# Performance work log

Measured on AMD Instinct MI355X. Metric: run time of the kernel, lower is better.

## Reference

```python
import jax, jax.numpy as jnp
import numpy as np

NEG_SLOPE = 0.2


def gat_conv(x, src, dst, W, att_src, att_dst, bias, heads, out_ch):
    # x: [N, Fin]; src/dst: [E] (self-loops already included)
    N = x.shape[0]
    h = (x @ W).reshape(N, heads, out_ch)                      # [N, H, C]
    a_s = jnp.einsum('nhc,hc->nh', h, att_src)                 # [N, H]
    a_d = jnp.einsum('nhc,hc->nh', h, att_dst)                 # [N, H]
    e = jax.nn.leaky_relu(a_s[src] + a_d[dst], NEG_SLOPE)      # [E, H]
    # segment softmax over incoming edges of each dst node
    e_max = jax.ops.segment_max(e, dst, num_segments=N)        # [N, H]
    p = jnp.exp(e - e_max[dst])                                # [E, H]
    denom = jax.ops.segment_sum(p, dst, num_segments=N)        # [N, H]
    alpha = p / denom[dst]                                     # [E, H]
    msg = h[src] * alpha[:, :, None]                           # [E, H, C]
    out = jax.ops.segment_sum(msg, dst, num_segments=N)        # [N, H, C]
    return out.reshape(N, heads * out_ch) + bias


def setup_inputs() -> dict:
    key = jax.random.key(0)
    ks = jax.random.split(key, 10)
    N, E, F_IN, HID, HEADS, NCLS = 100000, 3200000, 512, 8, 8, 16
    x = jax.random.normal(ks[0], (N, F_IN), dtype=jnp.float32)
    edge_index = jax.random.randint(ks[1], (2, E), 0, N, dtype=jnp.int64)
    s = 1.0 / np.sqrt(F_IN)
    W1 = jax.random.uniform(ks[2], (F_IN, HEADS * HID), jnp.float32, -s, s)
    att_src1 = jax.random.normal(ks[3], (HEADS, HID), jnp.float32) * 0.1
    att_dst1 = jax.random.normal(ks[4], (HEADS, HID), jnp.float32) * 0.1
    b1 = jnp.zeros((HEADS * HID,), jnp.float32)
    s2 = 1.0 / np.sqrt(HEADS * HID)
    W2 = jax.random.uniform(ks[5], (HEADS * HID, NCLS), jnp.float32, -s2, s2)
    att_src2 = jax.random.normal(ks[6], (1, NCLS), jnp.float32) * 0.1
    att_dst2 = jax.random.normal(ks[7], (1, NCLS), jnp.float32) * 0.1
    b2 = jnp.zeros((NCLS,), jnp.float32)
    return {"x": x, "edge_index": edge_index, "W1": W1, "att_src1": att_src1,
            "att_dst1": att_dst1, "b1": b1, "W2": W2, "att_src2": att_src2,
            "att_dst2": att_dst2, "b2": b2}


def reference(x, edge_index, W1, att_src1, att_dst1, b1, W2, att_src2, att_dst2, b2):
    N = x.shape[0]
    loops = jnp.arange(N, dtype=edge_index.dtype)
    src = jnp.concatenate([edge_index[0], loops])  # PyG add_self_loops=True
    dst = jnp.concatenate([edge_index[1], loops])
    # eval mode: F.dropout is identity
    h = gat_conv(x, src, dst, W1, att_src1, att_dst1, b1, heads=8, out_ch=8)
    h = jax.nn.elu(h)
    out = gat_conv(h, src, dst, W2, att_src2, att_dst2, b2, heads=1, out_ch=16)
    return out
```

## Files before the change

kernel.cpp:

```cpp
#include <hip/hip_runtime.h>

#define F_IN 512
#define F1 64
#define NCLS 16
#define NEG_SLOPE 0.2f

typedef __attribute__((ext_vector_type(8))) short short8;
typedef __attribute__((ext_vector_type(4))) float f32x4;

__device__ __forceinline__ unsigned short f2bf(float f) {
    unsigned u = __float_as_uint(f);
    return (unsigned short)((u + 0x7fffu + ((u >> 16) & 1u)) >> 16);
}
__device__ __forceinline__ float bf2f(unsigned short u) {
    return __uint_as_float(((unsigned)u) << 16);
}


__global__ __launch_bounds__(64) void k_detect(const int* __restrict__ ei, int E,
                                               unsigned* __restrict__ mode) {
    int t = threadIdx.x;
    unsigned nz = 0;
    int lim = (E > 256) ? 256 : E;
    for (int k = t; k < lim; k += 64) nz |= (unsigned)ei[2 * k + 1];
    for (int off = 1; off < 64; off <<= 1) nz |= __shfl_xor(nz, off);
    if (t == 0) *mode = (nz == 0) ? 1u : 0u;
}

__device__ __forceinline__ void decode_edge(const int* __restrict__ ei,
                                            const long long* __restrict__ e64,
                                            bool m64, unsigned i, int E, int N,
                                            int& s, int& v) {
    if (i < (unsigned)E) {
        if (m64) { s = (int)e64[i]; v = (int)e64[E + i]; }
        else     { s = ei[i];       v = ei[E + i]; }
    } else {
        s = (int)(i - (unsigned)E);
        v = s;
    }
    s = s < 0 ? 0 : (s >= N ? N - 1 : s);
    v = v < 0 ? 0 : (v >= N ? N - 1 : v);
}

__device__ __forceinline__ int decode_dst(const int* __restrict__ ei,
                                          const long long* __restrict__ e64,
                                          bool m64, unsigned i, int E, int N) {
    int v;
    if (i < (unsigned)E) v = m64 ? (int)e64[E + i] : ei[E + i];
    else                 v = (int)(i - (unsigned)E);
    return v < 0 ? 0 : (v >= N ? N - 1 : v);
}


__device__ __forceinline__ void gemm1_tile(const float* __restrict__ x,
                                           const float* __restrict__ W1,
                                           const float* __restrict__ att_s,
                                           const float* __restrict__ att_d,
                                           unsigned short* __restrict__ h1b,
                                           float* __restrict__ a_s1,
                                           float* __restrict__ a_d1,
                                           int N, int row0,
                                           unsigned short (*Abuf)[40],
                                           unsigned short (*BbufT)[40]) {
    const int tid = threadIdx.x;
    const int w = tid >> 6, lane = tid & 63;
    const int quad = lane >> 4, r16 = lane & 15;

    f32x4 acc[4];
#pragma unroll
    for (int t = 0; t < 4; t++) acc[t] = (f32x4){0.f, 0.f, 0.f, 0.f};

    const int a_row = tid >> 2;
    const int a_seg = (tid & 3) * 8;
    const int b_col = tid & 63;
    const int b_kq  = tid >> 6;
    const int ar = row0 + a_row;

    for (int k0 = 0; k0 < F_IN; k0 += 32) {
        {
            float4 v0 = make_float4(0.f, 0.f, 0.f, 0.f), v1 = v0;
            if (ar < N) {
                const float* xp = x + (size_t)ar * F_IN + k0 + a_seg;
                v0 = *(const float4*)xp;
                v1 = *(const float4*)(xp + 4);
            }
            short8 cv;
            cv[0] = (short)f2bf(v0.x); cv[1] = (short)f2bf(v0.y);
            cv[2] = (short)f2bf(v0.z); cv[3] = (short)f2bf(v0.w);
            cv[4] = (short)f2bf(v1.x); cv[5] = (short)f2bf(v1.y);
            cv[6] = (short)f2bf(v1.z); cv[7] = (short)f2bf(v1.w);
            *(short8*)&Abuf[a_row][a_seg] = cv;
        }
        {
            const float* wp = W1 + (size_t)(k0 + b_kq * 8) * F1 + b_col;
            short8 cv;
#pragma unroll
            for (int j = 0; j < 8; j++)
                cv[j] = (short)f2bf(wp[(size_t)j * F1]);
            *(short8*)&BbufT[b_col][b_kq * 8] = cv;
        }
        __syncthreads();

        short8 af = *(const short8*)&Abuf[w * 16 + r16][quad * 8];
#pragma unroll
        for (int t = 0; t < 4; t++) {
            short8 bf = *(const short8*)&BbufT[t * 16 + r16][quad * 8];
            acc[t] = __builtin_amdgcn_mfma_f32_16x16x32_bf16(af, bf, acc[t], 0, 0, 0);
        }
        __syncthreads();
    }

    float ats[4], atd[4];
#pragma unroll
    for (int t = 0; t < 4; t++) {
        ats[t] = att_s[t * 16 + r16];
        atd[t] = att_d[t * 16 + r16];
    }
#pragma unroll
    for (int r = 0; r < 4; r++) {
        int grow = row0 + w * 16 + quad * 4 + r;
        bool ok = grow < N;
        float ps[4], pd[4];
#pragma unroll
        for (int t = 0; t < 4; t++) {
            float vv = acc[t][r];
            if (ok) h1b[(size_t)grow * F1 + t * 16 + r16] = f2bf(vv);
            ps[t] = vv * ats[t];
            pd[t] = vv * atd[t];
        }
#pragma unroll
        for (int t = 0; t < 4; t++) {
            ps[t] += __shfl_xor(ps[t], 1); pd[t] += __shfl_xor(pd[t], 1);
            ps[t] += __shfl_xor(ps[t], 2); pd[t] += __shfl_xor(pd[t], 2);
            ps[t] += __shfl_xor(ps[t], 4); pd[t] += __shfl_xor(pd[t], 4);
        }
        if (ok && (r16 & 7) == 0) {
            int hh0 = r16 >> 3;
#pragma unroll
            for (int t = 0; t < 4; t++) {
                a_s1[(size_t)grow * 8 + t * 2 + hh0] = ps[t];
                a_d1[(size_t)grow * 8 + t * 2 + hh0] = pd[t];
            }
        }
    }
}


__global__ __launch_bounds__(256) void k_fusedA(const float* __restrict__ x,
                                                const float* __restrict__ W1,
                                                const float* __restrict__ att_s,
                                                const float* __restrict__ att_d,
                                                unsigned short* __restrict__ h1b,
                                                float* __restrict__ a_s1,
                                                float* __restrict__ a_d1, int N,
                                                const int* __restrict__ ei,
                                                const unsigned* __restrict__ mode,
                                                unsigned* __restrict__ bucketCnt,
                                                int E, int ET, int nch,
                                                int nb, int shift) {
    __shared__ __align__(16) char smem[10240];
    unsigned b = blockIdx.x;
    if ((b & 1) == 0) {
        gemm1_tile(x, W1, att_s, att_d, h1b, a_s1, a_d1, N, (int)(b >> 1) * 64,
                   (unsigned short (*)[40])smem,
                   (unsigned short (*)[40])(smem + 5120));
        return;
    }
    unsigned* cntL = (unsigned*)smem;
    for (int i = threadIdx.x; i < 1024; i += 256) cntL[i] = 0u;
    __syncthreads();

    const unsigned stride = (unsigned)nch * 256u;
    bool m64 = (*mode != 0u);
    const long long* e64 = (const long long*)ei;
    unsigned i = (b >> 1) * 256u + threadIdx.x;
    for (; i + 3u * stride < (unsigned)ET; i += 4u * stride) {
        int v0 = decode_dst(ei, e64, m64, i, E, N);
        int v1 = decode_dst(ei, e64, m64, i + stride, E, N);
        int v2 = decode_dst(ei, e64, m64, i + 2u * stride, E, N);
        int v3 = decode_dst(ei, e64, m64, i + 3u * stride, E, N);
        atomicAdd(&cntL[(unsigned)v0 >> shift], 1u);
        atomicAdd(&cntL[(unsigned)v1 >> shift], 1u);
        atomicAdd(&cntL[(unsigned)v2 >> shift], 1u);
        atomicAdd(&cntL[(unsigned)v3 >> shift], 1u);
    }
    for (; i < (unsigned)ET; i += stride) {
        int v = decode_dst(ei, e64, m64, i, E, N);
        atomicAdd(&cntL[(unsigned)v >> shift], 1u);
    }
    __syncthreads();
    for (int k = threadIdx.x; k < nb; k += 256) {
        unsigned c = cntL[k];
        if (c) atomicAdd(&bucketCnt[k], c);
    }
}


__global__ __launch_bounds__(256) void k_fusedB(const float* __restrict__ x,
                                                const float* __restrict__ W1,
                                                const float* __restrict__ att_s,
                                                const float* __restrict__ att_d,
                                                unsigned short* __restrict__ h1b,
                                                float* __restrict__ a_s1,
                                                float* __restrict__ a_d1, int N,
                                                int rowSplit,
                                                const int* __restrict__ ei,
                                                const unsigned* __restrict__ mode,
                                                unsigned* __restrict__ bucketFill,
                                                unsigned* __restrict__ pairs,
                                                int E, int ET, int nch,
                                                int nb, int shift) {
    __shared__ __align__(16) char smem[10240];
    unsigned b = blockIdx.x;
    if (b & 1) {
        gemm1_tile(x, W1, att_s, att_d, h1b, a_s1, a_d1, N,
                   rowSplit + (int)(b >> 1) * 64,
                   (unsigned short (*)[40])smem,
                   (unsigned short (*)[40])(smem + 5120));
        return;
    }
    unsigned* cntA = (unsigned*)smem;
    unsigned* ofsA = (unsigned*)(smem + 4096);
    unsigned* part = (unsigned*)(smem + 8192);
    const int t = threadIdx.x;
    const int chunk = (ET + nch - 1) / nch;
    const int cbase = (int)(b >> 1) * chunk;
    const int cend = (cbase + chunk < ET) ? cbase + chunk : ET;
    const unsigned lmask = (1u << shift) - 1u;
    bool m64 = (*mode != 0u);
    const long long* e64 = (const long long*)ei;

    for (int k = t; k < 1024; k += 256) cntA[k] = 0u;
    __syncthreads();
    for (int k = cbase + t; k < cend; k += 256) {
        int v = decode_dst(ei, e64, m64, (unsigned)k, E, N);
        atomicAdd(&cntA[(unsigned)v >> shift], 1u);
    }
    __syncthreads();
    unsigned a0 = cntA[4 * t + 0], a1 = cntA[4 * t + 1];
    unsigned a2 = cntA[4 * t + 2], a3 = cntA[4 * t + 3];
    unsigned ssum = a0 + a1 + a2 + a3;
    part[t] = ssum;
    __syncthreads();
    for (int off = 1; off < 256; off <<= 1) {
        unsigned add = (t >= off) ? part[t - off] : 0u;
        __syncthreads();
        part[t] += add;
        __syncthreads();
    }
    unsigned excl = part[t] - ssum;
    ofsA[4 * t + 0] = excl;
    ofsA[4 * t + 1] = excl + a0;
    ofsA[4 * t + 2] = excl + a0 + a1;
    ofsA[4 * t + 3] = excl + a0 + a1 + a2;
    __syncthreads();
    for (int k = t; k < nb; k += 256) {
        unsigned c = cntA[k];
        unsigned g = c ? atomicAdd(&bucketFill[k], c) : 0u;
        cntA[k] = g - ofsA[k];
    }
    __syncthreads();
    for (int k = cbase + t; k < cend; k += 256) {
        int s, v;
        decode_edge(ei, e64, m64, (unsigned)k, E, N, s, v);
        unsigned bb = (unsigned)v >> shift;
        unsigned slot = atomicAdd(&ofsA[bb], 1u);
        pairs[cntA[bb] + slot] = (unsigned)s | (((unsigned)v & lmask) << 20);
    }
}


__global__ __launch_bounds__(1024) void k_scan_buckets(const unsigned* __restrict__ bucketCnt,
                                                       int nb, int ET,
                                                       unsigned* __restrict__ bucketOfs,
                                                       unsigned* __restrict__ bucketFill,
                                                       unsigned* __restrict__ row_ptr,
                                                       int N) {
    __shared__ unsigned sbuf[1024];
    int t = threadIdx.x;
    unsigned val = (t < nb) ? bucketCnt[t] : 0u;
    sbuf[t] = val;
    __syncthreads();
    for (int off = 1; off < 1024; off <<= 1) {
        unsigned add = (t >= off) ? sbuf[t - off] : 0u;
        __syncthreads();
        sbuf[t] += add;
        __syncthreads();
    }
    if (t < nb) {
        unsigned e = sbuf[t] - val;
        bucketOfs[t] = e;
        bucketFill[t] = e;
    }
    if (t == 0) row_ptr[N] = (unsigned)ET;
}


__global__ __launch_bounds__(256) void k_sort(const unsigned* __restrict__ pairs,
                                              const unsigned* __restrict__ bucketOfs,
                                              const unsigned* __restrict__ bucketCnt,
                                              unsigned* __restrict__ row_ptr,
                                              unsigned* __restrict__ ssrc,
                                              int N, int shift) {
    __shared__ unsigned f[1024];
    __shared__ unsigned part[256];
    const int b = blockIdx.x;
    const int t = threadIdx.x;
    const int nodes = 1 << shift;
    const int bbase = b << shift;
    for (int i = t; i < 1024; i += 256) f[i] = 0u;
    __syncthreads();
    const unsigned base = bucketOfs[b];
    const unsigned cnt = bucketCnt[b];
    for (unsigned i = (unsigned)t; i < cnt; i += 256u)
        atomicAdd(&f[pairs[base + i] >> 20], 1u);
    __syncthreads();
    unsigned a0 = f[4 * t + 0], a1 = f[4 * t + 1];
    unsigned a2 = f[4 * t + 2], a3 = f[4 * t + 3];
    unsigned ssum = a0 + a1 + a2 + a3;
    part[t] = ssum;
    __syncthreads();
    for (int off = 1; off < 256; off <<= 1) {
        unsigned add = (t >= off) ? part[t - off] : 0u;
        __syncthreads();
        part[t] += add;
        __syncthreads();
    }
    unsigned excl = part[t] - ssum;
    unsigned c0 = base + excl;
    unsigned c1 = c0 + a0;
    unsigned c2 = c1 + a1;
    unsigned c3 = c2 + a2;
    {
        int v0 = bbase + 4 * t;
        if (v0 + 0 < N && 4 * t + 0 < nodes) row_ptr[v0 + 0] = c0;
        if (v0 + 1 < N && 4 * t + 1 < nodes) row_ptr[v0 + 1] = c1;
        if (v0 + 2 < N && 4 * t + 2 < nodes) row_ptr[v0 + 2] = c2;
        if (v0 + 3 < N && 4 * t + 3 < nodes) row_ptr[v0 + 3] = c3;
    }
    f[4 * t + 0] = c0;
    f[4 * t + 1] = c1;
    f[4 * t + 2] = c2;
    f[4 * t + 3] = c3;
    __syncthreads();
    for (unsigned i = (unsigned)t; i < cnt; i += 256u) {
        unsigned pk = pairs[base + i];
        unsigned local = pk >> 20;
        unsigned pos = atomicAdd(&f[local], 1u);
        ssrc[pos] = pk & 0xFFFFFu;
    }
}


__global__ __launch_bounds__(256) void k_agg1(const unsigned short* __restrict__ h1b,
                                              const float* __restrict__ a_s1,
                                              const float* __restrict__ a_d1,
                                              const float* __restrict__ b1,
                                              const unsigned* __restrict__ row_ptr,
                                              const unsigned* __restrict__ ssrc,
                                              float* __restrict__ g, int N) {
    int wid = threadIdx.x >> 6, lane = threadIdx.x & 63;
    int v = blockIdx.x * 4 + wid;
    if (v >= N) return;
    unsigned base = row_ptr[v];
    unsigned deg = row_ptr[v + 1] - base;
    int h = lane >> 3;
    float adv = a_d1[(size_t)v * 8 + h];

    float denom = 0.f, acc = 0.f;
    unsigned j = 0;
    for (; j + 8 <= deg; j += 8) {
        unsigned s0 = ssrc[base + j + 0];
        unsigned s1 = ssrc[base + j + 1];
        unsigned s2 = ssrc[base + j + 2];
        unsigned s3 = ssrc[base + j + 3];
        unsigned s4 = ssrc[base + j + 4];
        unsigned s5 = ssrc[base + j + 5];
        unsigned s6 = ssrc[base + j + 6];
        unsigned s7 = ssrc[base + j + 7];
        float as0 = a_s1[(size_t)s0 * 8 + h];
        float as1 = a_s1[(size_t)s1 * 8 + h];
        float as2 = a_s1[(size_t)s2 * 8 + h];
        float as3 = a_s1[(size_t)s3 * 8 + h];
        float as4 = a_s1[(size_t)s4 * 8 + h];
        float as5 = a_s1[(size_t)s5 * 8 + h];
        float as6 = a_s1[(size_t)s6 * 8 + h];
        float as7 = a_s1[(size_t)s7 * 8 + h];
        float h0 = bf2f(h1b[(size_t)s0 * F1 + lane]);
        float h1 = bf2f(h1b[(size_t)s1 * F1 + lane]);
        float h2v = bf2f(h1b[(size_t)s2 * F1 + lane]);
        float h3 = bf2f(h1b[(size_t)s3 * F1 + lane]);
        float h4 = bf2f(h1b[(size_t)s4 * F1 + lane]);
        float h5 = bf2f(h1b[(size_t)s5 * F1 + lane]);
        float h6 = bf2f(h1b[(size_t)s6 * F1 + lane]);
        float h7 = bf2f(h1b[(size_t)s7 * F1 + lane]);
        float e0 = as0 + adv; e0 = e0 > 0.f ? e0 : NEG_SLOPE * e0; float p0 = __expf(e0);
        float e1 = as1 + adv; e1 = e1 > 0.f ? e1 : NEG_SLOPE * e1; float p1 = __expf(e1);
        float e2 = as2 + adv; e2 = e2 > 0.f ? e2 : NEG_SLOPE * e2; float p2 = __expf(e2);
        float e3 = as3 + adv; e3 = e3 > 0.f ? e3 : NEG_SLOPE * e3; float p3 = __expf(e3);
        float e4 = as4 + adv; e4 = e4 > 0.f ? e4 : NEG_SLOPE * e4; float p4 = __expf(e4);
        float e5 = as5 + adv; e5 = e5 > 0.f ? e5 : NEG_SLOPE * e5; float p5 = __expf(e5);
        float e6 = as6 + adv; e6 = e6 > 0.f ? e6 : NEG_SLOPE * e6; float p6 = __expf(e6);
        float e7 = as7 + adv; e7 = e7 > 0.f ? e7 : NEG_SLOPE * e7; float p7 = __expf(e7);
        denom += ((p0 + p1) + (p2 + p3)) + ((p4 + p5) + (p6 + p7));
        acc = fmaf(h0, p0, acc);
        acc = fmaf(h1, p1, acc);
        acc = fmaf(h2v, p2, acc);
        acc = fmaf(h3, p3, acc);
        acc = fmaf(h4, p4, acc);
        acc = fmaf(h5, p5, acc);
        acc = fmaf(h6, p6, acc);
        acc = fmaf(h7, p7, acc);
    }
    for (; j < deg; j++) {
        unsigned s = ssrc[base + j];
        float as = a_s1[(size_t)s * 8 + h];
        float hv = bf2f(h1b[(size_t)s * F1 + lane]);
        float e = as + adv; e = e > 0.f ? e : NEG_SLOPE * e;
        float p = __expf(e);
        denom += p;
        acc = fmaf(hv, p, acc);
    }
    float t = acc * (1.0f / denom) + b1[lane];
    g[(size_t)v * F1 + lane] = t > 0.f ? t : (__expf(t) - 1.f);
}


__global__ __launch_bounds__(256) void k_gemm2(const float* __restrict__ g,
                                               const float* __restrict__ W2,
                                               const float* __restrict__ as2w,
                                               const float* __restrict__ ad2w,
                                               float* __restrict__ h2,
                                               float* __restrict__ a_s2,
                                               float* __restrict__ a_d2, int N) {
    __shared__ float W2s[F1][NCLS];
    int tid = threadIdx.x;
    for (int i = tid; i < F1 * NCLS; i += 256) ((float*)W2s)[i] = W2[i];
    __syncthreads();
    int lane = tid & 63, wid = tid >> 6;
    int n = blockIdx.x * 16 + wid * 4 + (lane >> 4);
    int c = lane & 15;
    if (n >= N) return;
    float acc = 0.f;
#pragma unroll
    for (int k4 = 0; k4 < 16; k4++) {
        float4 gv = *(const float4*)(g + (size_t)n * F1 + k4 * 4);
        acc = fmaf(gv.x, W2s[k4 * 4 + 0][c], acc);
        acc = fmaf(gv.y, W2s[k4 * 4 + 1][c], acc);
        acc = fmaf(gv.z, W2s[k4 * 4 + 2][c], acc);
        acc = fmaf(gv.w, W2s[k4 * 4 + 3][c], acc);
    }
    h2[(size_t)n * NCLS + c] = acc;
    float s = acc * as2w[c];
    float d = acc * ad2w[c];
    s += __shfl_xor(s, 1); s += __shfl_xor(s, 2); s += __shfl_xor(s, 4); s += __shfl_xor(s, 8);
    d += __shfl_xor(d, 1); d += __shfl_xor(d, 2); d += __shfl_xor(d, 4); d += __shfl_xor(d, 8);
    if (c == 0) { a_s2[n] = s; a_d2[n] = d; }
}


__global__ __launch_bounds__(256) void k_agg2(const float* __restrict__ h2,
                                              const float* __restrict__ a_s2,
                                              const float* __restrict__ a_d2,
                                              const float* __restrict__ b2,
                                              const unsigned* __restrict__ row_ptr,
                                              const unsigned* __restrict__ ssrc,
                                              float* __restrict__ out, int N) {
    int wid = threadIdx.x >> 6, lane = threadIdx.x & 63;
    int v = blockIdx.x * 4 + wid;
    if (v >= N) return;
    unsigned base = row_ptr[v];
    unsigned deg = row_ptr[v + 1] - base;
    float adv = a_d2[v];
    int sub = lane >> 4, c = lane & 15;

    float denom = 0.f, acc = 0.f;
    unsigned j = sub;
    for (; j + 12 < deg; j += 16) {
        unsigned s0 = ssrc[base + j + 0];
        unsigned s1 = ssrc[base + j + 4];
        unsigned s2 = ssrc[base + j + 8];
        unsigned s3 = ssrc[base + j + 12];
        float as0 = a_s2[s0];
        float as1 = a_s2[s1];
        float as2 = a_s2[s2];
        float as3 = a_s2[s3];
        float h0 = h2[(size_t)s0 * NCLS + c];
        float h1v = h2[(size_t)s1 * NCLS + c];
        float h2v = h2[(size_t)s2 * NCLS + c];
        float h3 = h2[(size_t)s3 * NCLS + c];
        float e0 = as0 + adv; e0 = e0 > 0.f ? e0 : NEG_SLOPE * e0; float p0 = __expf(e0);
        float e1 = as1 + adv; e1 = e1 > 0.f ? e1 : NEG_SLOPE * e1; float p1 = __expf(e1);
        float e2 = as2 + adv; e2 = e2 > 0.f ? e2 : NEG_SLOPE * e2; float p2 = __expf(e2);
        float e3 = as3 + adv; e3 = e3 > 0.f ? e3 : NEG_SLOPE * e3; float p3 = __expf(e3);
        denom += (p0 + p1) + (p2 + p3);
        acc = fmaf(h0, p0, acc);
        acc = fmaf(h1v, p1, acc);
        acc = fmaf(h2v, p2, acc);
        acc = fmaf(h3, p3, acc);
    }
    for (; j < deg; j += 4) {
        unsigned s = ssrc[base + j];
        float as = a_s2[s];
        float hv = h2[(size_t)s * NCLS + c];
        float e = as + adv; e = e > 0.f ? e : NEG_SLOPE * e;
        float p = __expf(e);
        denom += p;
        acc = fmaf(hv, p, acc);
    }
    acc += __shfl_xor(acc, 16);
    acc += __shfl_xor(acc, 32);
    denom += __shfl_xor(denom, 16);
    denom += __shfl_xor(denom, 32);
    if (lane < 16) {
        out[(size_t)v * NCLS + c] = acc * (1.0f / denom) + b2[c];
    }
}


static inline size_t algn(size_t x) { return (x + 255) & ~(size_t)255; }

extern "C" void kernel_launch(void* const* d_in, const int* in_sizes, int n_in,
                              void* d_out, int out_size, void* d_ws, size_t ws_size,
                              hipStream_t stream) {
    const float* x   = (const float*)d_in[0];
    const int* ei    = (const int*)d_in[1];
    const float* W1  = (const float*)d_in[2];
    const float* as1 = (const float*)d_in[3];
    const float* ad1 = (const float*)d_in[4];
    const float* b1  = (const float*)d_in[5];
    const float* W2  = (const float*)d_in[6];
    const float* as2 = (const float*)d_in[7];
    const float* ad2 = (const float*)d_in[8];
    const float* b2  = (const float*)d_in[9];

    const int N = in_sizes[0] / F_IN;
    const int E = in_sizes[1] / 2;
    const int ET = E + N;

    int shift = 8;
    int nb = (N + 255) >> 8;
    while (nb > 1024) { shift++; nb = (N + (1 << shift) - 1) >> shift; }

    const int GA_T = ((N / 2) + 63) / 64;
    const int rowSplit = GA_T * 64;
    const int GB_T = (N - rowSplit + 63) / 64;

    char* p = (char*)d_ws;
    unsigned short* h1b = (unsigned short*)p;  p += algn((size_t)N * F1 * 2);
    float* g    = (float*)p;      p += algn((size_t)N * F1 * 4);
    float* a_s1 = (float*)p;      p += algn((size_t)N * 8 * 4);
    float* a_d1 = (float*)p;      p += algn((size_t)N * 8 * 4);
    float* h2   = (float*)p;      p += algn((size_t)N * NCLS * 4);
    float* a_s2 = (float*)p;      p += algn((size_t)N * 4);
    float* a_d2 = (float*)p;      p += algn((size_t)N * 4);
    unsigned* row_ptr = (unsigned*)p;  p += algn((size_t)(N + 1) * 4);
    unsigned* bucketCnt  = (unsigned*)p;  p += algn((size_t)1024 * 4);
    unsigned* bucketOfs  = (unsigned*)p;  p += algn((size_t)1024 * 4);
    unsigned* bucketFill = (unsigned*)p;  p += algn((size_t)1024 * 4);
    unsigned* mode    = (unsigned*)p;  p += algn(256);
    unsigned* ssrc = (unsigned*)p;     p += algn((size_t)ET * 4);
    unsigned* pairs = (unsigned*)g;

    hipMemsetAsync(bucketCnt, 0, (size_t)nb * 4, stream);

    dim3 b256(256);
    k_detect<<<dim3(1), dim3(64), 0, stream>>>(ei, E, mode);

    k_fusedA<<<dim3(2 * GA_T), b256, 0, stream>>>(x, W1, as1, ad1, h1b, a_s1, a_d1, N,
                                                  ei, mode, bucketCnt,
                                                  E, ET, GA_T, nb, shift);

    k_scan_buckets<<<dim3(1), dim3(1024), 0, stream>>>(bucketCnt, nb, ET, bucketOfs,
                                                       bucketFill, row_ptr, N);

    k_fusedB<<<dim3(2 * GB_T), b256, 0, stream>>>(x, W1, as1, ad1, h1b, a_s1, a_d1, N,
                                                  rowSplit, ei, mode, bucketFill,
                                                  pairs, E, ET, GB_T, nb, shift);

    k_sort<<<dim3(nb), b256, 0, stream>>>(pairs, bucketOfs, bucketCnt, row_ptr, ssrc, N, shift);

    k_agg1<<<dim3((N + 3) / 4), b256, 0, stream>>>(h1b, a_s1, a_d1, b1, row_ptr, ssrc, g, N);
    k_gemm2<<<dim3((N + 15) / 16), b256, 0, stream>>>(g, W2, as2, ad2, h2, a_s2, a_d2, N);
    k_agg2<<<dim3((N + 3) / 4), b256, 0, stream>>>(h2, a_s2, a_d2, b2, row_ptr, ssrc,
                                                   (float*)d_out, N);
}
```

Measured before the change: 640.2 us.

## Pre-transpose W1 to bf16 and restructure layer-1 aggregation lane mapping

A new prep kernel converts W1 to a transposed bf16 copy once, so each GEMM tile loads B fragments with one 16-byte vector read instead of eight strided fp32 loads plus conversions. The layer-1 aggregation kernel is restructured so each lane computes one (edge, head) attention weight for 8 edges at a time and shares it via shuffles. Each half-wave then gathers packed bf16 pairs of features for alternating edges. This removes redundant per-lane exp/a_s loads and halves the feature-gather instruction count, at the cost of more shuffles, an extra tiny kernel launch, and idle lanes on low-degree nodes.

```diff
diff --git a/kernel.cpp b/kernel.cpp
--- a/kernel.cpp
+++ b/kernel.cpp
@@ -52,8 +52,18 @@
 }
 
 
+__global__ __launch_bounds__(256) void k_prep(const float* __restrict__ W1,
+                                              unsigned short* __restrict__ W1T) {
+    int t = blockIdx.x * 256 + threadIdx.x;
+    if (t < F_IN * F1) {
+        int k = t >> 6, c = t & 63;
+        W1T[(size_t)c * F_IN + k] = f2bf(W1[t]);
+    }
+}
+
+
 __device__ __forceinline__ void gemm1_tile(const float* __restrict__ x,
-                                           const float* __restrict__ W1,
+                                           const unsigned short* __restrict__ W1T,
                                            const float* __restrict__ att_s,
                                            const float* __restrict__ att_d,
                                            unsigned short* __restrict__ h1b,
@@ -92,12 +102,8 @@
             *(short8*)&Abuf[a_row][a_seg] = cv;
         }
         {
-            const float* wp = W1 + (size_t)(k0 + b_kq * 8) * F1 + b_col;
-            short8 cv;
-#pragma unroll
-            for (int j = 0; j < 8; j++)
-                cv[j] = (short)f2bf(wp[(size_t)j * F1]);
-            *(short8*)&BbufT[b_col][b_kq * 8] = cv;
+            const unsigned short* wp = W1T + (size_t)b_col * F_IN + k0 + b_kq * 8;
+            *(short8*)&BbufT[b_col][b_kq * 8] = *(const short8*)wp;
         }
         __syncthreads();
 
@@ -147,7 +153,7 @@
 
 
 __global__ __launch_bounds__(256) void k_fusedA(const float* __restrict__ x,
-                                                const float* __restrict__ W1,
+                                                const unsigned short* __restrict__ W1T,
                                                 const float* __restrict__ att_s,
                                                 const float* __restrict__ att_d,
                                                 unsigned short* __restrict__ h1b,
@@ -161,7 +167,7 @@
     __shared__ __align__(16) char smem[10240];
     unsigned b = blockIdx.x;
     if ((b & 1) == 0) {
-        gemm1_tile(x, W1, att_s, att_d, h1b, a_s1, a_d1, N, (int)(b >> 1) * 64,
+        gemm1_tile(x, W1T, att_s, att_d, h1b, a_s1, a_d1, N, (int)(b >> 1) * 64,
                    (unsigned short (*)[40])smem,
                    (unsigned short (*)[40])(smem + 5120));
         return;
@@ -197,7 +203,7 @@
 
 
 __global__ __launch_bounds__(256) void k_fusedB(const float* __restrict__ x,
-                                                const float* __restrict__ W1,
+                                                const unsigned short* __restrict__ W1T,
                                                 const float* __restrict__ att_s,
                                                 const float* __restrict__ att_d,
                                                 unsigned short* __restrict__ h1b,
@@ -213,7 +219,7 @@
     __shared__ __align__(16) char smem[10240];
     unsigned b = blockIdx.x;
     if (b & 1) {
-        gemm1_tile(x, W1, att_s, att_d, h1b, a_s1, a_d1, N,
+        gemm1_tile(x, W1T, att_s, att_d, h1b, a_s1, a_d1, N,
                    rowSplit + (int)(b >> 1) * 64,
                    (unsigned short (*)[40])smem,
                    (unsigned short (*)[40])(smem + 5120));
@@ -364,65 +370,49 @@
     if (v >= N) return;
     unsigned base = row_ptr[v];
     unsigned deg = row_ptr[v + 1] - base;
-    int h = lane >> 3;
-    float adv = a_d1[(size_t)v * 8 + h];
-
-    float denom = 0.f, acc = 0.f;
-    unsigned j = 0;
-    for (; j + 8 <= deg; j += 8) {
-        unsigned s0 = ssrc[base + j + 0];
-        unsigned s1 = ssrc[base + j + 1];
-        unsigned s2 = ssrc[base + j + 2];
-        unsigned s3 = ssrc[base + j + 3];
-        unsigned s4 = ssrc[base + j + 4];
-        unsigned s5 = ssrc[base + j + 5];
-        unsigned s6 = ssrc[base + j + 6];
-        unsigned s7 = ssrc[base + j + 7];
-        float as0 = a_s1[(size_t)s0 * 8 + h];
-        float as1 = a_s1[(size_t)s1 * 8 + h];
-        float as2 = a_s1[(size_t)s2 * 8 + h];
-        float as3 = a_s1[(size_t)s3 * 8 + h];
-        float as4 = a_s1[(size_t)s4 * 8 + h];
-        float as5 = a_s1[(size_t)s5 * 8 + h];
-        float as6 = a_s1[(size_t)s6 * 8 + h];
-        float as7 = a_s1[(size_t)s7 * 8 + h];
-        float h0 = bf2f(h1b[(size_t)s0 * F1 + lane]);
-        float h1 = bf2f(h1b[(size_t)s1 * F1 + lane]);
-        float h2v = bf2f(h1b[(size_t)s2 * F1 + lane]);
-        float h3 = bf2f(h1b[(size_t)s3 * F1 + lane]);
-        float h4 = bf2f(h1b[(size_t)s4 * F1 + lane]);
-        float h5 = bf2f(h1b[(size_t)s5 * F1 + lane]);
-        float h6 = bf2f(h1b[(size_t)s6 * F1 + lane]);
-        float h7 = bf2f(h1b[(size_t)s7 * F1 + lane]);
-        float e0 = as0 + adv; e0 = e0 > 0.f ? e0 : NEG_SLOPE * e0; float p0 = __expf(e0);
-        float e1 = as1 + adv; e1 = e1 > 0.f ? e1 : NEG_SLOPE * e1; float p1 = __expf(e1);
-        float e2 = as2 + adv; e2 = e2 > 0.f ? e2 : NEG_SLOPE * e2; float p2 = __expf(e2);
-        float e3 = as3 + adv; e3 = e3 > 0.f ? e3 : NEG_SLOPE * e3; float p3 = __expf(e3);
-        float e4 = as4 + adv; e4 = e4 > 0.f ? e4 : NEG_SLOPE * e4; float p4 = __expf(e4);
-        float e5 = as5 + adv; e5 = e5 > 0.f ? e5 : NEG_SLOPE * e5; float p5 = __expf(e5);
-        float e6 = as6 + adv; e6 = e6 > 0.f ? e6 : NEG_SLOPE * e6; float p6 = __expf(e6);
-        float e7 = as7 + adv; e7 = e7 > 0.f ? e7 : NEG_SLOPE * e7; float p7 = __expf(e7);
-        denom += ((p0 + p1) + (p2 + p3)) + ((p4 + p5) + (p6 + p7));
-        acc = fmaf(h0, p0, acc);
-        acc = fmaf(h1, p1, acc);
-        acc = fmaf(h2v, p2, acc);
-        acc = fmaf(h3, p3, acc);
-        acc = fmaf(h4, p4, acc);
-        acc = fmaf(h5, p5, acc);
-        acc = fmaf(h6, p6, acc);
-        acc = fmaf(h7, p7, acc);
-    }
-    for (; j < deg; j++) {
-        unsigned s = ssrc[base + j];
-        float as = a_s1[(size_t)s * 8 + h];
-        float hv = bf2f(h1b[(size_t)s * F1 + lane]);
-        float e = as + adv; e = e > 0.f ? e : NEG_SLOPE * e;
-        float p = __expf(e);
+
+    const int eA = lane >> 3, hA = lane & 7;
+    float adv = a_d1[(size_t)v * 8 + hA];
+    const int half = lane >> 5, j32 = lane & 31;
+    const int hq = j32 >> 2;
+
+    float denom = 0.f, acc0 = 0.f, acc1 = 0.f;
+    for (unsigned jj = 0; jj < deg; jj += 8) {
+        unsigned ee = jj + (unsigned)eA;
+        bool val = ee < deg;
+        unsigned sL = ssrc[base + (val ? ee : 0u)];
+        float as = a_s1[(size_t)sL * 8 + hA];
+        float eatt = as + adv;
+        eatt = eatt > 0.f ? eatt : NEG_SLOPE * eatt;
+        float p = val ? __expf(eatt) : 0.f;
         denom += p;
-        acc = fmaf(hv, p, acc);
-    }
-    float t = acc * (1.0f / denom) + b1[lane];
-    g[(size_t)v * F1 + lane] = t > 0.f ? t : (__expf(t) - 1.f);
+#pragma unroll
+        for (int k = 0; k < 4; k++) {
+            int esel = k * 2 + half;
+            unsigned s_my = (unsigned)__shfl((int)sL, esel * 8);
+            float p_my = __shfl(p, esel * 8 + hq);
+            unsigned u = *(const unsigned*)(h1b + ((size_t)s_my << 6) + (j32 << 1));
+            float lo = __uint_as_float(u << 16);
+            float hi = __uint_as_float(u & 0xffff0000u);
+            acc0 = fmaf(lo, p_my, acc0);
+            acc1 = fmaf(hi, p_my, acc1);
+        }
+    }
+    acc0 += __shfl_xor(acc0, 32);
+    acc1 += __shfl_xor(acc1, 32);
+    denom += __shfl_xor(denom, 8);
+    denom += __shfl_xor(denom, 16);
+    denom += __shfl_xor(denom, 32);
+    float dn = __shfl(denom, hq);
+    if (half == 0) {
+        float inv = 1.0f / dn;
+        int c0 = j32 * 2;
+        float t0 = acc0 * inv + b1[c0];
+        float t1 = acc1 * inv + b1[c0 + 1];
+        t0 = t0 > 0.f ? t0 : (__expf(t0) - 1.f);
+        t1 = t1 > 0.f ? t1 : (__expf(t1) - 1.f);
+        *(float2*)&g[(size_t)v * F1 + c0] = make_float2(t0, t1);
+    }
 }
 
 
@@ -559,6 +549,7 @@
     unsigned* bucketOfs  = (unsigned*)p;  p += algn((size_t)1024 * 4);
     unsigned* bucketFill = (unsigned*)p;  p += algn((size_t)1024 * 4);
     unsigned* mode    = (unsigned*)p;  p += algn(256);
+    unsigned short* W1T = (unsigned short*)p;  p += algn((size_t)F_IN * F1 * 2);
     unsigned* ssrc = (unsigned*)p;     p += algn((size_t)ET * 4);
     unsigned* pairs = (unsigned*)g;
 
@@ -566,15 +557,16 @@
 
     dim3 b256(256);
     k_detect<<<dim3(1), dim3(64), 0, stream>>>(ei, E, mode);
-
-    k_fusedA<<<dim3(2 * GA_T), b256, 0, stream>>>(x, W1, as1, ad1, h1b, a_s1, a_d1, N,
+    k_prep<<<dim3((F_IN * F1 + 255) / 256), b256, 0, stream>>>(W1, W1T);
+
+    k_fusedA<<<dim3(2 * GA_T), b256, 0, stream>>>(x, W1T, as1, ad1, h1b, a_s1, a_d1, N,
                                                   ei, mode, bucketCnt,
                                                   E, ET, GA_T, nb, shift);
 
     k_scan_buckets<<<dim3(1), dim3(1024), 0, stream>>>(bucketCnt, nb, ET, bucketOfs,
                                                        bucketFill, row_ptr, N);
 
-    k_fusedB<<<dim3(2 * GB_T), b256, 0, stream>>>(x, W1, as1, ad1, h1b, a_s1, a_d1, N,
+    k_fusedB<<<dim3(2 * GB_T), b256, 0, stream>>>(x, W1T, as1, ad1, h1b, a_s1, a_d1, N,
                                                   rowSplit, ei, mode, bucketFill,
                                                   pairs, E, ET, GB_T, nb, shift);
 
```

Result: no change. 631.7 us (-1.3%).
